# Optimization experiments

Measured on AMD Instinct MI355X. Metric: run time of the kernel, lower is better.

## Reference

```python
import jax, jax.numpy as jnp
import numpy as np

N, C, F, NB = 256, 4, 256, 32   # batch, in_channels, in_features, neighbors
OC, OF = 4, 256                 # out_channels, out_features


def setup_inputs() -> dict:
    key = jax.random.key(0)
    k1, k2, k3 = jax.random.split(key, 3)
    x = jax.random.normal(k1, (N, C, F), dtype=jnp.float32)
    neighbor = jax.random.normal(k2, (N, NB, C, F), dtype=jnp.float32)
    # Conv1d(in=2C, out=OC*OF, kernel_size=F, bias=False) weight
    W = jax.random.normal(k3, (OC * OF, 2 * C, F), dtype=jnp.float32) * 0.02
    return {"x": x, "neighbor": neighbor, "W": W}


def _feature_adjacency(x, neighbor):
    # batched version of per-sample einsum('ca,ncb->cab')
    fadj = jnp.einsum('Nca,Nncb->Ncab', x, neighbor)  # (N,C,F,F)
    fadj = fadj + jnp.swapaxes(fadj, -2, -1)
    # sign-sqrt
    s = jnp.sign(fadj) * jnp.sqrt(jnp.clip(jnp.abs(fadj), 1e-8, None))
    # row(col)-normalize over dim -2, then NaN mask
    adj = s / (jnp.abs(s).sum(-2, keepdims=True) + 1e-7)
    return jnp.where(jnp.isnan(adj), 0.0, adj)


def reference(x, neighbor, W):
    adj = _feature_adjacency(x, neighbor)            # (N,C,F,F)
    ax = jnp.einsum('Ncab,Ncb->Nca', adj, x)         # adj @ x
    xcat = jnp.concatenate([ax, x], axis=1)          # (N,2C,F)
    # Conv1d with kernel_size=F over length-F input == flat contraction
    out = jnp.einsum('Nif,oif->No', xcat, W).reshape(x.shape[0], OC, OF)
    return (out, adj)
```

## Files before the change

### kernel.cpp

```cpp
#include <hip/hip_runtime.h>
#include <math.h>

namespace {
constexpr int N_ = 256, C_ = 4, F_ = 256, NB_ = 32;
constexpr int O_ = 1024;
constexpr int OUT_ELEMS = N_ * O_;
constexpr int AX_ELEMS = N_ * C_ * F_;
constexpr int SPLITK = 16;
typedef float f32x4 __attribute__((ext_vector_type(4)));
}

__global__ __launch_bounds__(256) void adj_kernel(
    const float* __restrict__ x,
    const float* __restrict__ neighbor,
    float* __restrict__ adj,
    float* __restrict__ ax_out)
{
  __shared__ float4 xsw[F_];
  __shared__ float red[4][F_];
  const int blk = blockIdx.x;
  const int n = blk >> 2, c = blk & 3;
  const int t = threadIdx.x;
  const int rs = t >> 6;
  const int lane = t & 63;
  const int b0 = lane * 4;

  const int base = (n * C_ + c) * F_;
  {
    const float xv = x[base + t];
    const float* p = neighbor + ((size_t)(n * NB_) * C_ + c) * F_ + t;
    float s = 0.f;
    #pragma unroll
    for (int j = 0; j < NB_; ++j) s += p[(size_t)j * C_ * F_];
    xsw[t] = make_float4(xv, s, 0.f, 0.f);
  }
  __syncthreads();

  float xbv[4], sbv[4];
  #pragma unroll
  for (int j = 0; j < 4; ++j) {
    const float4 q = xsw[b0 + j];
    xbv[j] = q.x;
    sbv[j] = q.y;
  }

  float cs[4] = {0.f, 0.f, 0.f, 0.f};
  const int a0r = rs * 64;
  #pragma unroll 4
  for (int a = a0r; a < a0r + 64; ++a) {
    const float2 xs = *(const float2*)&xsw[a];
    const float xa = xs.x, sa = xs.y;
    #pragma unroll
    for (int j = 0; j < 4; ++j) {
      float v = fmaf(xa, sbv[j], xbv[j] * sa);
      float m = fmaxf(fabsf(v), 1e-8f);
      float rq = __builtin_amdgcn_rsqf(m);
      cs[j] = fmaf(fabsf(v), rq, cs[j]);
    }
  }
  *(float4*)&red[rs][b0] = make_float4(cs[0], cs[1], cs[2], cs[3]);
  __syncthreads();

  float invv[4];
  {
    const float4 r0 = *(const float4*)&red[0][b0];
    const float4 r1 = *(const float4*)&red[1][b0];
    const float4 r2 = *(const float4*)&red[2][b0];
    const float4 r3 = *(const float4*)&red[3][b0];
    invv[0] = 1.f / (r0.x + r1.x + r2.x + r3.x + 1e-7f);
    invv[1] = 1.f / (r0.y + r1.y + r2.y + r3.y + 1e-7f);
    invv[2] = 1.f / (r0.z + r1.z + r2.z + r3.z + 1e-7f);
    invv[3] = 1.f / (r0.w + r1.w + r2.w + r3.w + 1e-7f);
  }
  if (rs == 0) {
    #pragma unroll
    for (int j = 0; j < 4; ++j) xsw[b0 + j].z = invv[j] * xbv[j];
  }
  __syncthreads();

  float axp[4] = {0.f, 0.f, 0.f, 0.f};
  float* arow = adj + (size_t)(n * C_ + c) * (F_ * F_);
  #pragma unroll 4
  for (int a = a0r; a < a0r + 64; ++a) {
    const float4 q = xsw[a];
    const float xa = q.x, sa = q.y, wa = q.z;
    float o[4];
    #pragma unroll
    for (int j = 0; j < 4; ++j) {
      float v = fmaf(xa, sbv[j], xbv[j] * sa);
      float m = fmaxf(fabsf(v), 1e-8f);
      float rq = __builtin_amdgcn_rsqf(m);
      float tt = v * rq;
      o[j] = tt * invv[j];
      axp[j] = fmaf(tt, wa, axp[j]);
    }
    f32x4 ov = {o[0], o[1], o[2], o[3]};
    __builtin_nontemporal_store(ov, (f32x4*)&arow[(size_t)a * F_ + b0]);
  }
  *(float4*)&red[rs][b0] = make_float4(axp[0], axp[1], axp[2], axp[3]);
  __syncthreads();
  if (rs == 0) {
    const float4 r0 = *(const float4*)&red[0][b0];
    const float4 r1 = *(const float4*)&red[1][b0];
    const float4 r2 = *(const float4*)&red[2][b0];
    const float4 r3 = *(const float4*)&red[3][b0];
    const float4 axv = make_float4(r0.x + r1.x + r2.x + r3.x,
                                   r0.y + r1.y + r2.y + r3.y,
                                   r0.z + r1.z + r2.z + r3.z,
                                   r0.w + r1.w + r2.w + r3.w);
    *(float4*)&ax_out[base + b0] = axv;
  }
}

namespace {
constexpr int TM = 128, TO = 128, BK = 32, PL = 144;
__device__ __forceinline__ int swz(int c) { return c + ((c >> 5) << 2); }
}

template <bool USE_WS>
__global__ __launch_bounds__(256) void gemm_kernel(
    const float* __restrict__ ax,
    const float* __restrict__ x,
    const float* __restrict__ W,
    float* __restrict__ dst)
{
  __shared__ float As[BK * PL];
  __shared__ float Bs[BK * PL];
  const int tid = threadIdx.x;
  const int m0 = blockIdx.x * TM, o0 = blockIdx.y * TO;
  const int kbeg = blockIdx.z * 128;
  const float* Ab = (kbeg < 1024) ? ax + kbeg : x + (kbeg - 1024);

  const int sr = tid >> 1;
  const int kq = (tid & 1) * 16;
  const int psr = swz(sr);
  const int mi = tid >> 4, oi = tid & 15;
  const int pa = swz(mi * 8), pb = swz(oi * 8);

  const float* Arow = Ab + (size_t)(m0 + sr) * 1024 + kq;
  const float* Brow = W + (size_t)(o0 + sr) * 2048 + kbeg + kq;

  float4 ra[4], rb[4];
  #pragma unroll
  for (int q = 0; q < 4; ++q) {
    ra[q] = *(const float4*)&Arow[q * 4];
    rb[q] = *(const float4*)&Brow[q * 4];
  }

  float acc[8][8] = {};

  for (int tt = 0; tt < 4; ++tt) {
    #pragma unroll
    for (int q = 0; q < 4; ++q) {
      const float av[4] = {ra[q].x, ra[q].y, ra[q].z, ra[q].w};
      const float bv[4] = {rb[q].x, rb[q].y, rb[q].z, rb[q].w};
      #pragma unroll
      for (int e = 0; e < 4; ++e) {
        As[(kq + q * 4 + e) * PL + psr] = av[e];
        Bs[(kq + q * 4 + e) * PL + psr] = bv[e];
      }
    }
    __syncthreads();
    if (tt < 3) {
      #pragma unroll
      for (int q = 0; q < 4; ++q) {
        ra[q] = *(const float4*)&Arow[(tt + 1) * BK + q * 4];
        rb[q] = *(const float4*)&Brow[(tt + 1) * BK + q * 4];
      }
    }
    #pragma unroll 8
    for (int kk = 0; kk < BK; ++kk) {
      const float4 a0 = *(const float4*)&As[kk * PL + pa];
      const float4 a1 = *(const float4*)&As[kk * PL + pa + 4];
      const float4 b0 = *(const float4*)&Bs[kk * PL + pb];
      const float4 b1 = *(const float4*)&Bs[kk * PL + pb + 4];
      const float am[8] = {a0.x, a0.y, a0.z, a0.w, a1.x, a1.y, a1.z, a1.w};
      const float bm[8] = {b0.x, b0.y, b0.z, b0.w, b1.x, b1.y, b1.z, b1.w};
      #pragma unroll
      for (int i = 0; i < 8; ++i)
        #pragma unroll
        for (int j = 0; j < 8; ++j)
          acc[i][j] = fmaf(am[i], bm[j], acc[i][j]);
    }
    __syncthreads();
  }

  if (USE_WS) {
    float* p = dst + (size_t)blockIdx.z * OUT_ELEMS;
    #pragma unroll
    for (int i = 0; i < 8; ++i) {
      float* prow = &p[(size_t)(m0 + mi * 8 + i) * 1024 + o0 + oi * 8];
      *(float4*)&prow[0] = make_float4(acc[i][0], acc[i][1], acc[i][2], acc[i][3]);
      *(float4*)&prow[4] = make_float4(acc[i][4], acc[i][5], acc[i][6], acc[i][7]);
    }
  } else {
    #pragma unroll
    for (int i = 0; i < 8; ++i) {
      float* orow = &dst[(size_t)(m0 + mi * 8 + i) * 1024 + o0 + oi * 8];
      #pragma unroll
      for (int j = 0; j < 8; ++j) atomicAdd(&orow[j], acc[i][j]);
    }
  }
}

__global__ __launch_bounds__(256) void reduce_kernel(
    const float* __restrict__ parts, float* __restrict__ out) {
  const int i = (blockIdx.x * 256 + threadIdx.x) * 4;
  float4 s = make_float4(0.f, 0.f, 0.f, 0.f);
  #pragma unroll
  for (int z = 0; z < SPLITK; ++z) {
    const float4 v = *(const float4*)&parts[(size_t)z * OUT_ELEMS + i];
    s.x += v.x; s.y += v.y; s.z += v.z; s.w += v.w;
  }
  f32x4 sv = {s.x, s.y, s.z, s.w};
  __builtin_nontemporal_store(sv, (f32x4*)&out[i]);
}

extern "C" void kernel_launch(void* const* d_in, const int* in_sizes, int n_in,
                              void* d_out, int out_size, void* d_ws,
                              size_t ws_size, hipStream_t stream) {
  const float* x = (const float*)d_in[0];
  const float* neighbor = (const float*)d_in[1];
  const float* W = (const float*)d_in[2];
  float* out = (float*)d_out;
  float* adj = out + OUT_ELEMS;
  float* ax = (float*)d_ws;

  adj_kernel<<<dim3(N_ * C_), dim3(256), 0, stream>>>(x, neighbor, adj, ax);

  const size_t need = (size_t)(AX_ELEMS + SPLITK * OUT_ELEMS) * sizeof(float);
  if (ws_size >= need) {
    float* parts = ax + AX_ELEMS;
    gemm_kernel<true><<<dim3(256 / TM, O_ / TO, SPLITK), dim3(256), 0, stream>>>(
        ax, x, W, parts);
    reduce_kernel<<<dim3(OUT_ELEMS / (256 * 4)), dim3(256), 0, stream>>>(parts,
                                                                         out);
  } else {
    (void)hipMemsetAsync(out, 0, OUT_ELEMS * sizeof(float), stream);
    gemm_kernel<false><<<dim3(256 / TM, O_ / TO, SPLITK), dim3(256), 0, stream>>>(
        ax, x, W, out);
  }
}
```

Baseline: 321.0 us.

## Split adjacency kernel into colsum and store passes; retile GEMM to 64x128

The fused adjacency kernel becomes two kernels. The first computes neighbor sums and the column normalisers and packs x, s, inv*x and inv per feature into workspace. The second reloads that packed data and only streams the normalised adjacency and the ax reduction, so the write-heavy pass no longer sits behind the column-sum phase inside each block. The split-K GEMM moves from 128x128 tiles with 256 threads to 64x128 tiles with 128 threads, doubling the block count, with new padded shared-memory strides. The cost is an extra launch and a round trip of the packed array through global memory.

```diff
diff --git a/kernel.cpp b/kernel.cpp
--- a/kernel.cpp
+++ b/kernel.cpp
@@ -6,25 +6,144 @@
 constexpr int O_ = 1024;
 constexpr int OUT_ELEMS = N_ * O_;
 constexpr int AX_ELEMS = N_ * C_ * F_;
+constexpr int ROWS = N_ * C_;
 constexpr int SPLITK = 16;
 typedef float f32x4 __attribute__((ext_vector_type(4)));
 }
 
-__global__ __launch_bounds__(256) void adj_kernel(
+__global__ __launch_bounds__(256) void colsum_kernel(
     const float* __restrict__ x,
     const float* __restrict__ neighbor,
+    float4* __restrict__ packed)
+{
+  __shared__ float2 xs2[F_];
+  __shared__ float red[4][F_];
+  __shared__ float invl[F_];
+  const int blk = blockIdx.x;
+  const int n = blk >> 2, c = blk & 3;
+  const int t = threadIdx.x;
+  const int rs = t >> 6, lane = t & 63, b0 = lane * 4;
+  const int base = blk * F_;
+
+  float xv, sv;
+  {
+    xv = x[base + t];
+    const float* p = neighbor + ((size_t)(n * NB_) * C_ + c) * F_ + t;
+    float s = 0.f;
+    #pragma unroll
+    for (int j = 0; j < NB_; ++j) s += p[(size_t)j * C_ * F_];
+    sv = s;
+    xs2[t] = make_float2(xv, s);
+  }
+  __syncthreads();
+
+  float xbv[4], sbv[4];
+  #pragma unroll
+  for (int j = 0; j < 4; ++j) {
+    const float2 q = xs2[b0 + j];
+    xbv[j] = q.x;
+    sbv[j] = q.y;
+  }
+
+  float cs[4] = {0.f, 0.f, 0.f, 0.f};
+  const int a0r = rs * 64;
+  #pragma unroll 4
+  for (int a = a0r; a < a0r + 64; ++a) {
+    const float2 xs = xs2[a];
+    const float xa = xs.x, sa = xs.y;
+    #pragma unroll
+    for (int j = 0; j < 4; ++j) {
+      float v = fmaf(xa, sbv[j], xbv[j] * sa);
+      float m = fmaxf(fabsf(v), 1e-8f);
+      float rq = __builtin_amdgcn_rsqf(m);
+      cs[j] = fmaf(fabsf(v), rq, cs[j]);
+    }
+  }
+  *(float4*)&red[rs][b0] = make_float4(cs[0], cs[1], cs[2], cs[3]);
+  __syncthreads();
+
+  if (rs == 0) {
+    const float4 r0 = *(const float4*)&red[0][b0];
+    const float4 r1 = *(const float4*)&red[1][b0];
+    const float4 r2 = *(const float4*)&red[2][b0];
+    const float4 r3 = *(const float4*)&red[3][b0];
+    invl[b0 + 0] = 1.f / (r0.x + r1.x + r2.x + r3.x + 1e-7f);
+    invl[b0 + 1] = 1.f / (r0.y + r1.y + r2.y + r3.y + 1e-7f);
+    invl[b0 + 2] = 1.f / (r0.z + r1.z + r2.z + r3.z + 1e-7f);
+    invl[b0 + 3] = 1.f / (r0.w + r1.w + r2.w + r3.w + 1e-7f);
+  }
+  __syncthreads();
+  const float inv = invl[t];
+  packed[base + t] = make_float4(xv, sv, inv * xv, inv);
+}
+
+__global__ __launch_bounds__(256) void adj_store_kernel(
+    const float4* __restrict__ packed,
     float* __restrict__ adj,
     float* __restrict__ ax_out)
 {
   __shared__ float4 xsw[F_];
   __shared__ float red[4][F_];
   const int blk = blockIdx.x;
+  const int t = threadIdx.x;
+  const int rs = t >> 6, lane = t & 63, b0 = lane * 4;
+
+  xsw[t] = packed[blk * F_ + t];
+  __syncthreads();
+
+  float xbv[4], sbv[4], invv[4];
+  #pragma unroll
+  for (int j = 0; j < 4; ++j) {
+    const float4 q = xsw[b0 + j];
+    xbv[j] = q.x;
+    sbv[j] = q.y;
+    invv[j] = q.w;
+  }
+
+  float axp[4] = {0.f, 0.f, 0.f, 0.f};
+  float* arow = adj + (size_t)blk * (F_ * F_);
+  const int a0r = rs * 64;
+  #pragma unroll 4
+  for (int a = a0r; a < a0r + 64; ++a) {
+    const float4 q = xsw[a];
+    const float xa = q.x, sa = q.y, wa = q.z;
+    float o[4];
+    #pragma unroll
+    for (int j = 0; j < 4; ++j) {
+      float v = fmaf(xa, sbv[j], xbv[j] * sa);
+      float m = fmaxf(fabsf(v), 1e-8f);
+      float rq = __builtin_amdgcn_rsqf(m);
+      float tt = v * rq;
+      o[j] = tt * invv[j];
+      axp[j] = fmaf(tt, wa, axp[j]);
+    }
+    f32x4 ov = {o[0], o[1], o[2], o[3]};
+    __builtin_nontemporal_store(ov, (f32x4*)&arow[(size_t)a * F_ + b0]);
+  }
+  *(float4*)&red[rs][b0] = make_float4(axp[0], axp[1], axp[2], axp[3]);
+  __syncthreads();
+  if (rs == 0) {
+    const float4 r0 = *(const float4*)&red[0][b0];
+    const float4 r1 = *(const float4*)&red[1][b0];
+    const float4 r2 = *(const float4*)&red[2][b0];
+    const float4 r3 = *(const float4*)&red[3][b0];
+    const float4 axv = make_float4(r0.x + r1.x + r2.x + r3.x,
+                                   r0.y + r1.y + r2.y + r3.y,
+                                   r0.z + r1.z + r2.z + r3.z,
+                                   r0.w + r1.w + r2.w + r3.w);
+    *(float4*)&ax_out[blk * F_ + b0] = axv;
+  }
+}
+
+__global__ __launch_bounds__(256) void adj_kernel(
+    const float* __restrict__ x, const float* __restrict__ neighbor,
+    float* __restrict__ adj, float* __restrict__ ax_out) {
+  __shared__ float4 xsw[F_];
+  __shared__ float red[4][F_];
+  const int blk = blockIdx.x;
   const int n = blk >> 2, c = blk & 3;
   const int t = threadIdx.x;
-  const int rs = t >> 6;
-  const int lane = t & 63;
-  const int b0 = lane * 4;
-
+  const int rs = t >> 6, lane = t & 63, b0 = lane * 4;
   const int base = (n * C_ + c) * F_;
   {
     const float xv = x[base + t];
@@ -35,7 +154,6 @@
     xsw[t] = make_float4(xv, s, 0.f, 0.f);
   }
   __syncthreads();
-
   float xbv[4], sbv[4];
   #pragma unroll
   for (int j = 0; j < 4; ++j) {
@@ -43,7 +161,6 @@
     xbv[j] = q.x;
     sbv[j] = q.y;
   }
-
   float cs[4] = {0.f, 0.f, 0.f, 0.f};
   const int a0r = rs * 64;
   #pragma unroll 4
@@ -60,7 +177,6 @@
   }
   *(float4*)&red[rs][b0] = make_float4(cs[0], cs[1], cs[2], cs[3]);
   __syncthreads();
-
   float invv[4];
   {
     const float4 r0 = *(const float4*)&red[0][b0];
@@ -77,7 +193,6 @@
     for (int j = 0; j < 4; ++j) xsw[b0 + j].z = invv[j] * xbv[j];
   }
   __syncthreads();
-
   float axp[4] = {0.f, 0.f, 0.f, 0.f};
   float* arow = adj + (size_t)(n * C_ + c) * (F_ * F_);
   #pragma unroll 4
@@ -104,48 +219,45 @@
     const float4 r1 = *(const float4*)&red[1][b0];
     const float4 r2 = *(const float4*)&red[2][b0];
     const float4 r3 = *(const float4*)&red[3][b0];
-    const float4 axv = make_float4(r0.x + r1.x + r2.x + r3.x,
-                                   r0.y + r1.y + r2.y + r3.y,
-                                   r0.z + r1.z + r2.z + r3.z,
-                                   r0.w + r1.w + r2.w + r3.w);
-    *(float4*)&ax_out[base + b0] = axv;
+    *(float4*)&ax_out[base + b0] = make_float4(
+        r0.x + r1.x + r2.x + r3.x, r0.y + r1.y + r2.y + r3.y,
+        r0.z + r1.z + r2.z + r3.z, r0.w + r1.w + r2.w + r3.w);
   }
 }
 
 namespace {
-constexpr int TM = 128, TO = 128, BK = 32, PL = 144;
+constexpr int TM2 = 64, TO2 = 128, BK = 32;
+constexpr int PLA = 68, PLB = 140;
 __device__ __forceinline__ int swz(int c) { return c + ((c >> 5) << 2); }
 }
 
 template <bool USE_WS>
-__global__ __launch_bounds__(256) void gemm_kernel(
+__global__ __launch_bounds__(128) void gemm_kernel(
     const float* __restrict__ ax,
     const float* __restrict__ x,
     const float* __restrict__ W,
     float* __restrict__ dst)
 {
-  __shared__ float As[BK * PL];
-  __shared__ float Bs[BK * PL];
+  __shared__ float As[BK * PLA];
+  __shared__ float Bs[BK * PLB];
   const int tid = threadIdx.x;
-  const int m0 = blockIdx.x * TM, o0 = blockIdx.y * TO;
+  const int m0 = blockIdx.x * TM2, o0 = blockIdx.y * TO2;
   const int kbeg = blockIdx.z * 128;
   const float* Ab = (kbeg < 1024) ? ax + kbeg : x + (kbeg - 1024);
 
-  const int sr = tid >> 1;
-  const int kq = (tid & 1) * 16;
-  const int psr = swz(sr);
+  const int sr8 = tid >> 3;
+  const int kq = (tid & 7) * 4;
   const int mi = tid >> 4, oi = tid & 15;
   const int pa = swz(mi * 8), pb = swz(oi * 8);
 
-  const float* Arow = Ab + (size_t)(m0 + sr) * 1024 + kq;
-  const float* Brow = W + (size_t)(o0 + sr) * 2048 + kbeg + kq;
-
-  float4 ra[4], rb[4];
-  #pragma unroll
-  for (int q = 0; q < 4; ++q) {
-    ra[q] = *(const float4*)&Arow[q * 4];
-    rb[q] = *(const float4*)&Brow[q * 4];
-  }
+  const float* Arow = Ab + (size_t)(m0 + sr8) * 1024 + kq;
+  const float* Brow = W + (size_t)(o0 + sr8) * 2048 + kbeg + kq;
+
+  float4 ra[4], rb[8];
+  #pragma unroll
+  for (int q = 0; q < 4; ++q) ra[q] = *(const float4*)&Arow[(size_t)q * 16 * 1024];
+  #pragma unroll
+  for (int q = 0; q < 8; ++q) rb[q] = *(const float4*)&Brow[(size_t)q * 16 * 2048];
 
   float acc[8][8] = {};
 
@@ -153,27 +265,32 @@
     #pragma unroll
     for (int q = 0; q < 4; ++q) {
       const float av[4] = {ra[q].x, ra[q].y, ra[q].z, ra[q].w};
+      const int pr = swz(sr8 + 16 * q);
+      #pragma unroll
+      for (int e = 0; e < 4; ++e) As[(kq + e) * PLA + pr] = av[e];
+    }
+    #pragma unroll
+    for (int q = 0; q < 8; ++q) {
       const float bv[4] = {rb[q].x, rb[q].y, rb[q].z, rb[q].w};
-      #pragma unroll
-      for (int e = 0; e < 4; ++e) {
-        As[(kq + q * 4 + e) * PL + psr] = av[e];
-        Bs[(kq + q * 4 + e) * PL + psr] = bv[e];
-      }
+      const int pr = swz(sr8 + 16 * q);
+      #pragma unroll
+      for (int e = 0; e < 4; ++e) Bs[(kq + e) * PLB + pr] = bv[e];
     }
     __syncthreads();
     if (tt < 3) {
       #pragma unroll
-      for (int q = 0; q < 4; ++q) {
-        ra[q] = *(const float4*)&Arow[(tt + 1) * BK + q * 4];
-        rb[q] = *(const float4*)&Brow[(tt + 1) * BK + q * 4];
-      }
+      for (int q = 0; q < 4; ++q)
+        ra[q] = *(const float4*)&Arow[(tt + 1) * BK + (size_t)q * 16 * 1024];
+      #pragma unroll
+      for (int q = 0; q < 8; ++q)
+        rb[q] = *(const float4*)&Brow[(tt + 1) * BK + (size_t)q * 16 * 2048];
     }
     #pragma unroll 8
     for (int kk = 0; kk < BK; ++kk) {
-      const float4 a0 = *(const float4*)&As[kk * PL + pa];
-      const float4 a1 = *(const float4*)&As[kk * PL + pa + 4];
-      const float4 b0 = *(const float4*)&Bs[kk * PL + pb];
-      const float4 b1 = *(const float4*)&Bs[kk * PL + pb + 4];
+      const float4 a0 = *(const float4*)&As[kk * PLA + pa];
+      const float4 a1 = *(const float4*)&As[kk * PLA + pa + 4];
+      const float4 b0 = *(const float4*)&Bs[kk * PLB + pb];
+      const float4 b1 = *(const float4*)&Bs[kk * PLB + pb + 4];
       const float am[8] = {a0.x, a0.y, a0.z, a0.w, a1.x, a1.y, a1.z, a1.w};
       const float bm[8] = {b0.x, b0.y, b0.z, b0.w, b1.x, b1.y, b1.z, b1.w};
       #pragma unroll
@@ -226,18 +343,20 @@
   float* adj = out + OUT_ELEMS;
   float* ax = (float*)d_ws;
 
-  adj_kernel<<<dim3(N_ * C_), dim3(256), 0, stream>>>(x, neighbor, adj, ax);
-
   const size_t need = (size_t)(AX_ELEMS + SPLITK * OUT_ELEMS) * sizeof(float);
   if (ws_size >= need) {
+    float4* packed = (float4*)(ax + AX_ELEMS);
     float* parts = ax + AX_ELEMS;
-    gemm_kernel<true><<<dim3(256 / TM, O_ / TO, SPLITK), dim3(256), 0, stream>>>(
-        ax, x, W, parts);
+    colsum_kernel<<<dim3(ROWS), dim3(256), 0, stream>>>(x, neighbor, packed);
+    adj_store_kernel<<<dim3(ROWS), dim3(256), 0, stream>>>(packed, adj, ax);
+    gemm_kernel<true><<<dim3(256 / TM2, O_ / TO2, SPLITK), dim3(128), 0,
+                        stream>>>(ax, x, W, parts);
     reduce_kernel<<<dim3(OUT_ELEMS / (256 * 4)), dim3(256), 0, stream>>>(parts,
                                                                          out);
   } else {
+    adj_kernel<<<dim3(ROWS), dim3(256), 0, stream>>>(x, neighbor, adj, ax);
     (void)hipMemsetAsync(out, 0, OUT_ELEMS * sizeof(float), stream);
-    gemm_kernel<false><<<dim3(256 / TM, O_ / TO, SPLITK), dim3(256), 0, stream>>>(
-        ax, x, W, out);
-  }
-}
+    gemm_kernel<false><<<dim3(256 / TM2, O_ / TO2, SPLITK), dim3(128), 0,
+                         stream>>>(ax, x, W, out);
+  }
+}
```

Result: slower. 336.0 us (+4.7%).
